# Kernel optimization log

Hardware: AMD Instinct MI355X
Metric: run time of the kernel (lower is better)

The kernel has to match this reference:

```python
import jax, jax.numpy as jnp
import numpy as np

WINDOW_SIZE = 11
SIGMA = 1.5
CHANNEL = 3
L = 2.0
C1 = (0.01 * L) ** 2
C2 = (0.03 * L) ** 2
WEIGHTS = jnp.asarray([0.0448, 0.2856, 0.3001, 0.2363, 0.1333], dtype=jnp.float32)


def _create_window(window_size=WINDOW_SIZE, channel=CHANNEL):
    x = jnp.arange(window_size, dtype=jnp.float32)
    g = jnp.exp(-((x - window_size // 2) ** 2) / (2.0 * SIGMA ** 2))
    g = g / g.sum()
    w2d = jnp.outer(g, g)  # (ws, ws)
    # depthwise kernel, OIHW with I=1, O=channel
    return jnp.broadcast_to(w2d[None, None], (channel, 1, window_size, window_size))


def _depthwise_conv(x, w):
    # x: (B,C,H,W), w: (C,1,kh,kw), groups=C, VALID padding
    return jax.lax.conv_general_dilated(
        x, w, window_strides=(1, 1), padding='VALID',
        feature_group_count=x.shape[1],
        dimension_numbers=('NCHW', 'OIHW', 'NCHW'))


def _ssim_level(img1, img2, window):
    mu1 = _depthwise_conv(img1, window)
    mu2 = _depthwise_conv(img2, window)
    mu1_sq = mu1 * mu1
    mu2_sq = mu2 * mu2
    mu1_mu2 = mu1 * mu2
    sigma1_sq = _depthwise_conv(img1 * img1, window) - mu1_sq
    sigma2_sq = _depthwise_conv(img2 * img2, window) - mu2_sq
    sigma12 = _depthwise_conv(img1 * img2, window) - mu1_mu2
    v1 = 2.0 * sigma12 + C2
    v2 = sigma1_sq + sigma2_sq + C2
    cs = jnp.mean(v1 / v2)
    ssim_map = (2.0 * mu1_mu2 + C1) * v1 / ((mu1_sq + mu2_sq + C1) * v2)
    return jnp.mean(ssim_map), cs


def _avg_pool2(x):
    b, c, h, w = x.shape
    return x.reshape(b, c, h // 2, 2, w // 2, 2).mean(axis=(3, 5))


def _msssim(img1, img2):
    window = _create_window()
    mssim, mcs = [], []
    for _ in range(WEIGHTS.shape[0]):
        sim, cs = _ssim_level(img1, img2, window)
        mssim.append(sim)
        mcs.append(cs)
        img1 = _avg_pool2(img1)
        img2 = _avg_pool2(img2)
    mssim = jnp.stack(mssim)
    mcs = jnp.stack(mcs)
    # normalize=True
    mssim = (mssim + 1.0) / 2.0
    mcs = (mcs + 1.0) / 2.0
    pow1 = mcs ** WEIGHTS
    pow2 = mssim ** WEIGHTS
    # faithful to source: prod over broadcast of pow1[:-1] * pow2[-1]
    return jnp.prod(pow1[:-1] * pow2[-1])


def setup_inputs() -> dict:
    key = jax.random.key(0)
    k1, k2 = jax.random.split(key)
    shape = (16, 3, 512, 512)
    output = jax.random.uniform(k1, shape, dtype=jnp.float32)
    gt = jax.random.uniform(k2, shape, dtype=jnp.float32)
    return {"output": output, "gt": gt}


def reference(output, gt):
    return 1.0 - _msssim(output, gt)
```

## Files before the change

### kernel.cpp

```cpp
#include <hip/hip_runtime.h>
#include <math.h>

typedef float vf2 __attribute__((ext_vector_type(2)));

__device__ __forceinline__ vf2 pk_fma(vf2 a, vf2 b, vf2 c) {
    vf2 d;
    asm("v_pk_fma_f32 %0, %1, %2, %3" : "=v"(d) : "v"(a), "v"(b), "v"(c));
    return d;
}
__device__ __forceinline__ vf2 pk_mul(vf2 a, vf2 b) {
    vf2 d;
    asm("v_pk_mul_f32 %0, %1, %2" : "=v"(d) : "v"(a), "v"(b));
    return d;
}
__device__ __forceinline__ vf2 pk_fma_blo(vf2 w, vf2 b, vf2 c) {
    vf2 d;
    asm("v_pk_fma_f32 %0, %1, %2, %3 op_sel_hi:[0,1,1]"
        : "=v"(d) : "v"(w), "v"(b), "v"(c));
    return d;
}
__device__ __forceinline__ vf2 pk_fma_bhi(vf2 w, vf2 b, vf2 c) {
    vf2 d;
    asm("v_pk_fma_f32 %0, %1, %2, %3 op_sel:[1,0,0] op_sel_hi:[1,1,1]"
        : "=v"(d) : "v"(w), "v"(b), "v"(c));
    return d;
}

#define L0_H 512
#define L0_HOUT 502
#define L0_SEG 64
#define L0_NCHUNK 7
#define ROWW 536
#define NQ 134
#define L0_BUF (11 * ROWW)

#define TILE 32
#define IN_DIM 42
#define SCP 21
#define HALO 10
#define LV_STAGE (IN_DIM * SCP * 4)
#define SH 340
#define HB LV_STAGE
#define MEGA_WORDS (HB + 16 * SH)

__global__ __launch_bounds__(256)
void msssim_cascade(const float* __restrict__ img1, const float* __restrict__ img2,
                    float* __restrict__ Y1, float* __restrict__ Y2,
                    float* __restrict__ Z1, float* __restrict__ Z2,
                    float* __restrict__ W1, float* __restrict__ W2)
{
    __shared__ float xs[16 * 256 * 2];
    __shared__ float ysh[8 * 128 * 2];
    __shared__ float zsh[4 * 64 * 2];
    const int tid = threadIdx.x;
    const int reg = blockIdx.x & 15, plane = blockIdx.x >> 4;
    const long long obase = (long long)plane * 262144;

    for (int i = tid; i < 16 * 256; i += 256) {
        const int r = i >> 8, c = i & 255;
        const long long o = obase + (long long)(2 * (16 * reg + r)) * 512 + 2 * c;
        const float2 a0 = *(const float2*)&img1[o];
        const float2 a1 = *(const float2*)&img1[o + 512];
        const float2 b0 = *(const float2*)&img2[o];
        const float2 b1 = *(const float2*)&img2[o + 512];
        xs[2 * i]     = 0.25f * ((a0.x + b0.x) + (a0.y + b0.y) + (a1.x + b1.x) + (a1.y + b1.y));
        xs[2 * i + 1] = 0.25f * ((a0.x - b0.x) + (a0.y - b0.y) + (a1.x - b1.x) + (a1.y - b1.y));
    }
    __syncthreads();
    for (int i = tid; i < 8 * 128; i += 256) {
        const int r = i >> 7, c = i & 127;
        const int i00 = ((2 * r) * 256 + 2 * c) * 2;
        const float yP = 0.25f * (xs[i00] + xs[i00 + 2] + xs[i00 + 512] + xs[i00 + 514]);
        const float yQ = 0.25f * (xs[i00 + 1] + xs[i00 + 3] + xs[i00 + 513] + xs[i00 + 515]);
        ysh[2 * i] = yP; ysh[2 * i + 1] = yQ;
        const long long yo = (long long)plane * 16384 + (long long)(8 * reg + r) * 128 + c;
        Y1[yo] = yP; Y2[yo] = yQ;
    }
    __syncthreads();
    for (int i = tid; i < 4 * 64; i += 256) {
        const int r = i >> 6, c = i & 63;
        const int i00 = ((2 * r) * 128 + 2 * c) * 2;
        const float zP = 0.25f * (ysh[i00] + ysh[i00 + 2] + ysh[i00 + 256] + ysh[i00 + 258]);
        const float zQ = 0.25f * (ysh[i00 + 1] + ysh[i00 + 3] + ysh[i00 + 257] + ysh[i00 + 259]);
        zsh[2 * i] = zP; zsh[2 * i + 1] = zQ;
        const long long zo = (long long)plane * 4096 + (long long)(4 * reg + r) * 64 + c;
        Z1[zo] = zP; Z2[zo] = zQ;
    }
    __syncthreads();
    for (int i = tid; i < 2 * 32; i += 256) {
        const int r = i >> 5, c = i & 31;
        const int i00 = ((2 * r) * 64 + 2 * c) * 2;
        const long long wo = (long long)plane * 1024 + (long long)(2 * reg + r) * 32 + c;
        W1[wo] = 0.25f * (zsh[i00] + zsh[i00 + 2] + zsh[i00 + 128] + zsh[i00 + 130]);
        W2[wo] = 0.25f * (zsh[i00 + 1] + zsh[i00 + 3] + zsh[i00 + 129] + zsh[i00 + 131]);
    }
}

__global__ __launch_bounds__(256)
void msssim_mega(const float* __restrict__ img1, const float* __restrict__ img2,
                 const float* __restrict__ Y1, const float* __restrict__ Y2,
                 const float* __restrict__ Z1, const float* __restrict__ Z2,
                 const float* __restrict__ W1, const float* __restrict__ W2,
                 double* __restrict__ sums)
{
    __shared__ __align__(16) float smem[MEGA_WORDS];
    __shared__ float wred[4][2];

    const float gs[11] = {0.00102838f, 0.00759875f, 0.03600077f, 0.10936070f,
                          0.21300554f, 0.26601173f, 0.21300554f, 0.10936070f,
                          0.03600077f, 0.00759875f, 0.00102838f};
    const int tid = threadIdx.x;
    const int bid = blockIdx.x;
    const float C1 = 4.0e-4f, C2 = 3.6e-3f;
    float ssim_acc = 0.f, cs_acc = 0.f;
    int level;

    if (bid < 768) {
        level = 0;
        const int c0 = (bid & 1) * 256;
        const int oy0 = ((bid >> 1) & 7) * L0_SEG;
        const long long plane = (long long)(bid >> 4) * 262144;
        const bool colok = (c0 + tid) < L0_HOUT;

        const int par = tid & 1;
        vf2 wp[6];
        #pragma unroll
        for (int jq = 0; jq < 6; ++jq) {
            const int i0 = 2 * jq, i1 = 2 * jq + 1;
            const float we0 = (i0 < 11) ? gs[i0] : 0.f;
            const float wo0 = (i0 >= 1) ? gs[i0 - 1] : 0.f;
            const float we1 = (i1 < 11) ? gs[i1] : 0.f;
            const float wo1 = (i1 >= 1) ? gs[i1 - 1] : 0.f;
            wp[jq].x = par ? wo0 : we0;
            wp[jq].y = par ? wo1 : we1;
        }
        vf2 wgv[6];
        #pragma unroll
        for (int k = 0; k < 6; ++k) { wgv[k].x = gs[k]; wgv[k].y = gs[k]; }

        int rowS[6], colS[6], ldsoff[6], rHS[6];
        #pragma unroll
        for (int t = 0; t < 6; ++t) {
            const int s = tid + 256 * t;
            if (s < 11 * NQ) {
                const int r = s / NQ, q = s - NQ * r;
                rowS[t] = r; colS[t] = c0 + 2 * q;
                ldsoff[t] = r * ROWW + q * 4; rHS[t] = r * L0_H;
            } else { rowS[t] = -1; colS[t] = 0; ldsoff[t] = 0; rHS[t] = 0; }
        }

        float4 pf[6];
        auto prefetch = [&](int ybase) {
            const int yH = ybase * L0_H;
            #pragma unroll
            for (int t = 0; t < 6; ++t) {
                float2 a = make_float2(0.f, 0.f), b = make_float2(0.f, 0.f);
                if (rowS[t] >= 0) {
                    const int y = ybase + rowS[t];
                    if (y < L0_H && colS[t] < L0_H) {
                        const long long idx = plane + yH + rHS[t] + colS[t];
                        a = *(const float2*)(img1 + idx);
                        b = *(const float2*)(img2 + idx);
                    }
                }
                pf[t] = make_float4(a.x + b.x, a.x - b.x, a.y + b.y, a.y - b.y);
            }
        };
        auto stage_write = [&]() {
            #pragma unroll
            for (int t = 0; t < 6; ++t)
                if (rowS[t] >= 0) *(float4*)&smem[ldsoff[t]] = pf[t];
        };

        prefetch(oy0);
        stage_write();
        __syncthreads();

        vf2 pd_pq[11], pd_sq[11];
        #pragma unroll
        for (int s = 0; s < 11; ++s) { pd_pq[s] = (vf2){0.f, 0.f}; pd_sq[s] = (vf2){0.f, 0.f}; }

        const int qb4 = (tid >> 1) * 4;

        for (int c = 0; c < L0_NCHUNK; ++c) {
            const bool more = (c + 1 < L0_NCHUNK);
            if (more) prefetch(oy0 + 11 * (c + 1));

            #pragma unroll
            for (int j = 0; j < 11; ++j) {
                pd_pq[j] = (vf2){0.f, 0.f};
                pd_sq[j] = (vf2){0.f, 0.f};

                float4 q[6];
                const int rw = j * ROWW + qb4;
                #pragma unroll
                for (int u = 0; u < 6; ++u) q[u] = *(const float4*)&smem[rw + 4 * u];

                vf2 hpq = {0.f, 0.f}, hsq = {0.f, 0.f};
                #pragma unroll
                for (int u = 0; u < 6; ++u) {
                    const vf2 elo = {q[u].x, q[u].y};
                    const vf2 ehi = {q[u].z, q[u].w};
                    const vf2 slo = pk_mul(elo, elo);
                    const vf2 shi = pk_mul(ehi, ehi);
                    hpq = pk_fma_blo(wp[u], elo, hpq);
                    hpq = pk_fma_bhi(wp[u], ehi, hpq);
                    hsq = pk_fma_blo(wp[u], slo, hsq);
                    hsq = pk_fma_bhi(wp[u], shi, hsq);
                }
                #pragma unroll
                for (int k = 0; k < 11; ++k) {
                    const int s = (j - k + 11) % 11;
                    const int m = (k <= 5) ? k : 10 - k;
                    pd_pq[s] = pk_fma(wgv[m], hpq, pd_pq[s]);
                    pd_sq[s] = pk_fma(wgv[m], hsq, pd_sq[s]);
                }
                const int yrel = 11 * c + j;
                if (yrel >= 10) {
                    const int s = (j + 1) % 11;
                    const int orow = yrel - 10;
                    if (orow < L0_SEG && (oy0 + orow) < L0_HOUT && colok) {
                        const vf2 musq = pk_mul(pd_pq[s], pd_pq[s]);
                        const float sP = pd_sq[s].x - musq.x;
                        const float sQ = pd_sq[s].y - musq.y;
                        const float v1 = 0.5f * (sP - sQ) + C2;
                        const float v2 = 0.5f * (sP + sQ) + C2;
                        const float num1 = 0.5f * (musq.x - musq.y) + C1;
                        const float den1 = 0.5f * (musq.x + musq.y) + C1;
                        cs_acc += v1 * __builtin_amdgcn_rcpf(v2);
                        ssim_acc += num1 * v1 * __builtin_amdgcn_rcpf(den1 * v2);
                    }
                }
            }

            __syncthreads();
            if (more) stage_write();
            __syncthreads();
        }
    } else {
        const int id = bid - 768;
        const float *src1 = nullptr, *src2 = nullptr;
        int H, strip, seg, plane, tps;
        if (id < 768) {
            level = 1; H = 256; tps = 4;
            plane = id >> 4; const int t = id & 15; strip = t & 7; seg = t >> 3;
        } else if (id < 1536) {
            level = 2; H = 128; tps = 1; src1 = Y1; src2 = Y2;
            const int r = id - 768; plane = r >> 4; const int t = r & 15; strip = t & 3; seg = t >> 2;
        } else if (id < 1728) {
            level = 3; H = 64; tps = 1; src1 = Z1; src2 = Z2;
            const int r = id - 1536; plane = r >> 2; const int t = r & 3; strip = t & 1; seg = t >> 1;
        } else {
            level = 4; H = 32; tps = 1; src1 = W1; src2 = W2;
            plane = id - 1728; strip = 0; seg = 0;
        }

        vf2 wg[11];
        #pragma unroll
        for (int k = 0; k < 11; ++k) { wg[k].x = gs[k]; wg[k].y = gs[k]; }

        const int Hout = H - HALO;
        const int ntiles = (Hout + TILE - 1) / TILE;
        const int tstart = seg * tps;
        const int tend = min(ntiles, tstart + tps);
        const int ox0 = strip * TILE;
        const long long base = (long long)plane * H * H;
        const long long obase = (long long)plane * 262144;

        int rHS[4], rS[4], xS[4];
        #pragma unroll
        for (int t4 = 0; t4 < 4; ++t4) {
            const int s = tid + 256 * t4;
            if (s < IN_DIM * SCP) {
                const int r = s / SCP, cp = s - r * SCP;
                rS[t4] = r; rHS[t4] = r * H; xS[t4] = ox0 + 2 * cp;
            } else { rS[t4] = -1; rHS[t4] = 0; xS[t4] = 0; }
        }

        auto load_slot = [&](int t4, int ybase) -> float4 {
            if (rS[t4] < 0) return make_float4(0.f, 0.f, 0.f, 0.f);
            const int y = ybase + rS[t4], x = xS[t4];
            if (y >= H || x >= H) return make_float4(0.f, 0.f, 0.f, 0.f);
            if (level == 1) {
                const long long o = obase + (long long)(2 * y) * 512 + 2 * x;
                const float4 A0 = *(const float4*)(img1 + o);
                const float4 A1 = *(const float4*)(img1 + o + 512);
                const float4 B0 = *(const float4*)(img2 + o);
                const float4 B1 = *(const float4*)(img2 + o + 512);
                const float P0 = 0.25f * ((A0.x + B0.x) + (A0.y + B0.y) + (A1.x + B1.x) + (A1.y + B1.y));
                const float Q0 = 0.25f * ((A0.x - B0.x) + (A0.y - B0.y) + (A1.x - B1.x) + (A1.y - B1.y));
                const float P1 = 0.25f * ((A0.z + B0.z) + (A0.w + B0.w) + (A1.z + B1.z) + (A1.w + B1.w));
                const float Q1 = 0.25f * ((A0.z - B0.z) + (A0.w - B0.w) + (A1.z - B1.z) + (A1.w - B1.w));
                return make_float4(P0, Q0, P1, Q1);
            }
            const long long idx = base + (long long)ybase * H + rHS[t4] + x;
            const float2 a = *(const float2*)(src1 + idx);
            const float2 b = *(const float2*)(src2 + idx);
            return make_float4(a.x, b.x, a.y, b.y);
        };

        float4 pref[4];
        {
            #pragma unroll
            for (int t4 = 0; t4 < 4; ++t4) pref[t4] = load_slot(t4, tstart * TILE);
            #pragma unroll
            for (int t4 = 0; t4 < 4; ++t4)
                if (rS[t4] >= 0) *(float4*)&smem[(tid + 256 * t4) * 4] = pref[t4];
        }
        __syncthreads();

        for (int tt = tstart; tt < tend; ++tt) {
            const int ty0 = tt * TILE;
            const bool more = (tt + 1 < tend);

            if (more) {
                #pragma unroll
                for (int t4 = 0; t4 < 4; ++t4) pref[t4] = load_slot(t4, ty0 + TILE);
            }

            float4 hA[3], hBv[3];
            #pragma unroll
            for (int t = 0; t < 3; ++t) {
                const int p = tid + 256 * t;
                if (p < IN_DIM * 16) {
                    const int r = p >> 4, m = p & 15;
                    vf2 Apq = {0.f, 0.f}, Asq = {0.f, 0.f};
                    vf2 Bpq = {0.f, 0.f}, Bsq = {0.f, 0.f};
                    #pragma unroll
                    for (int jj = 0; jj < 6; ++jj) {
                        const float4 v = *(const float4*)&smem[(r * SCP + m + jj) * 4];
                        const vf2 lo = {v.x, v.y};
                        const vf2 hi = {v.z, v.w};
                        const vf2 losq = pk_mul(lo, lo);
                        const vf2 hisq = pk_mul(hi, hi);
                        Apq = pk_fma(wg[2 * jj], lo, Apq);
                        Asq = pk_fma(wg[2 * jj], losq, Asq);
                        if (jj >= 1) {
                            Bpq = pk_fma(wg[2 * jj - 1], lo, Bpq);
                            Bsq = pk_fma(wg[2 * jj - 1], losq, Bsq);
                        }
                        if (jj <= 4) {
                            Apq = pk_fma(wg[2 * jj + 1], hi, Apq);
                            Asq = pk_fma(wg[2 * jj + 1], hisq, Asq);
                        }
                        Bpq = pk_fma(wg[2 * jj], hi, Bpq);
                        Bsq = pk_fma(wg[2 * jj], hisq, Bsq);
                    }
                    hA[t]  = make_float4(Apq.x, Apq.y, Asq.x, Asq.y);
                    hBv[t] = make_float4(Bpq.x, Bpq.y, Bsq.x, Bsq.y);
                }
            }
            __syncthreads();

            #pragma unroll
            for (int t = 0; t < 3; ++t) {
                const int p = tid + 256 * t;
                if (p < IN_DIM * 16) {
                    const int r = p >> 4, m = p & 15;
                    const int hb = HB + m * SH + r * 8;
                    *(float4*)&smem[hb]     = hA[t];
                    *(float4*)&smem[hb + 4] = hBv[t];
                }
            }
            if (more) {
                #pragma unroll
                for (int t4 = 0; t4 < 4; ++t4)
                    if (rS[t4] >= 0) *(float4*)&smem[(tid + 256 * t4) * 4] = pref[t4];
            }
            __syncthreads();

            const int tx = tid & 31, rg = tid >> 5;
            const int r0 = rg * 4;
            const int m = tx >> 1, par = tx & 1;
            const int hb = HB + m * SH + par * 4;

            vf2 accPQ[4], accSQ[4];
            #pragma unroll
            for (int o = 0; o < 4; ++o) {
                accPQ[o] = (vf2){0.f, 0.f};
                accSQ[o] = (vf2){0.f, 0.f};
            }
            #pragma unroll
            for (int i = 0; i < 14; ++i) {
                const float4 h4 = *(const float4*)&smem[hb + (r0 + i) * 8];
                const vf2 ppq = {h4.x, h4.y};
                const vf2 psq = {h4.z, h4.w};
                #pragma unroll
                for (int o = 0; o < 4; ++o) {
                    const int k = i - o;
                    if (k >= 0 && k <= 10) {
                        accPQ[o] = pk_fma(wg[k], ppq, accPQ[o]);
                        accSQ[o] = pk_fma(wg[k], psq, accSQ[o]);
                    }
                }
            }

            const int ox = ox0 + tx;
            #pragma unroll
            for (int o = 0; o < 4; ++o) {
                const int oy = ty0 + r0 + o;
                if (oy < Hout && ox < Hout) {
                    const vf2 musq = pk_mul(accPQ[o], accPQ[o]);
                    const float sP = accSQ[o].x - musq.x;
                    const float sQ = accSQ[o].y - musq.y;
                    const float v1 = 0.5f * (sP - sQ) + C2;
                    const float v2 = 0.5f * (sP + sQ) + C2;
                    const float num1 = 0.5f * (musq.x - musq.y) + C1;
                    const float den1 = 0.5f * (musq.x + musq.y) + C1;
                    cs_acc += v1 * __builtin_amdgcn_rcpf(v2);
                    ssim_acc += num1 * v1 * __builtin_amdgcn_rcpf(den1 * v2);
                }
            }
        }
    }

    #pragma unroll
    for (int off = 32; off > 0; off >>= 1) {
        ssim_acc += __shfl_down(ssim_acc, off);
        cs_acc   += __shfl_down(cs_acc, off);
    }
    const int wave = tid >> 6;
    if ((tid & 63) == 0) { wred[wave][0] = ssim_acc; wred[wave][1] = cs_acc; }
    __syncthreads();
    if (tid == 0) {
        const float s = wred[0][0] + wred[1][0] + wred[2][0] + wred[3][0];
        const float c = wred[0][1] + wred[1][1] + wred[2][1] + wred[3][1];
        atomicAdd(&sums[level],     (double)s);
        atomicAdd(&sums[5 + level], (double)c);
    }
}

__global__ void msssim_final_kernel(const double* __restrict__ sums,
                                    float* __restrict__ out)
{
    if (threadIdx.x == 0 && blockIdx.x == 0) {
        const double W[5] = {0.0448, 0.2856, 0.3001, 0.2363, 0.1333};
        const int Houts[5] = {502, 246, 118, 54, 22};
        double mssim[5], mcs[5];
        for (int l = 0; l < 5; ++l) {
            const double cnt = 48.0 * (double)Houts[l] * (double)Houts[l];
            mssim[l] = (sums[l]     / cnt + 1.0) * 0.5;
            mcs[l]   = (sums[5 + l] / cnt + 1.0) * 0.5;
        }
        const double p2 = pow(mssim[4], W[4]);
        double prod = 1.0;
        for (int l = 0; l < 4; ++l) prod *= pow(mcs[l], W[l]) * p2;
        out[0] = (float)(1.0 - prod);
    }
}

extern "C" void kernel_launch(void* const* d_in, const int* in_sizes, int n_in,
                              void* d_out, int out_size, void* d_ws, size_t ws_size,
                              hipStream_t stream)
{
    const float* img1 = (const float*)d_in[0];
    const float* img2 = (const float*)d_in[1];
    float* out = (float*)d_out;
    (void)in_sizes; (void)n_in; (void)out_size; (void)ws_size;

    char* ws = (char*)d_ws;
    double* sums = (double*)ws;
    float* Y1 = (float*)(ws + 256);
    float* Y2 = Y1 + 786432;
    float* Z1 = Y2 + 786432;
    float* Z2 = Z1 + 196608;
    float* W1 = Z2 + 196608;
    float* W2 = W1 + 49152;

    hipMemsetAsync(sums, 0, 10 * sizeof(double), stream);

    hipLaunchKernelGGL(msssim_cascade, dim3(768), dim3(256), 0, stream,
                       img1, img2, Y1, Y2, Z1, Z2, W1, W2);

    hipLaunchKernelGGL(msssim_mega, dim3(2544), dim3(256), 0, stream,
                       img1, img2, Y1, Y2, Z1, Z2, W1, W2, sums);

    hipLaunchKernelGGL(msssim_final_kernel, dim3(1), dim3(64), 0, stream, sums, out);
}
```

Baseline: 129.8 us.

## Materialize level-1 pooled images and process level 1 with streaming row kernel

The cascade kernel now also writes the level-1 pooled P/Q planes (X1/X2) to workspace. The mega kernel's level-1 work then leaves the 32x32 tiled path, which re-pooled from the full-resolution images, and runs through the streaming row-chunk path used for level 0, parameterized by H, Hout and source. This removes redundant full-resolution reads and tile halo overhead for level 1 and cuts the grid size. The cost is an extra ~25MB of global writes and reads for X1/X2, and the prefetch double-buffering in the tiled path is dropped.

```diff
diff --git a/kernel.cpp b/kernel.cpp
--- a/kernel.cpp
+++ b/kernel.cpp
@@ -26,13 +26,11 @@
     return d;
 }
 
-#define L0_H 512
-#define L0_HOUT 502
 #define L0_SEG 64
-#define L0_NCHUNK 7
+#define NCHUNK 7
 #define ROWW 536
 #define NQ 134
-#define L0_BUF (11 * ROWW)
+#define STREAM_BUF (11 * ROWW)
 
 #define TILE 32
 #define IN_DIM 42
@@ -45,6 +43,7 @@
 
 __global__ __launch_bounds__(256)
 void msssim_cascade(const float* __restrict__ img1, const float* __restrict__ img2,
+                    float* __restrict__ X1, float* __restrict__ X2,
                     float* __restrict__ Y1, float* __restrict__ Y2,
                     float* __restrict__ Z1, float* __restrict__ Z2,
                     float* __restrict__ W1, float* __restrict__ W2)
@@ -63,8 +62,11 @@
         const float2 a1 = *(const float2*)&img1[o + 512];
         const float2 b0 = *(const float2*)&img2[o];
         const float2 b1 = *(const float2*)&img2[o + 512];
-        xs[2 * i]     = 0.25f * ((a0.x + b0.x) + (a0.y + b0.y) + (a1.x + b1.x) + (a1.y + b1.y));
-        xs[2 * i + 1] = 0.25f * ((a0.x - b0.x) + (a0.y - b0.y) + (a1.x - b1.x) + (a1.y - b1.y));
+        const float P = 0.25f * ((a0.x + b0.x) + (a0.y + b0.y) + (a1.x + b1.x) + (a1.y + b1.y));
+        const float Q = 0.25f * ((a0.x - b0.x) + (a0.y - b0.y) + (a1.x - b1.x) + (a1.y - b1.y));
+        xs[2 * i] = P; xs[2 * i + 1] = Q;
+        const long long xo = (long long)plane * 65536 + (long long)(16 * reg + r) * 256 + c;
+        X1[xo] = P; X2[xo] = Q;
     }
     __syncthreads();
     for (int i = tid; i < 8 * 128; i += 256) {
@@ -98,6 +100,7 @@
 
 __global__ __launch_bounds__(256)
 void msssim_mega(const float* __restrict__ img1, const float* __restrict__ img2,
+                 const float* __restrict__ X1, const float* __restrict__ X2,
                  const float* __restrict__ Y1, const float* __restrict__ Y2,
                  const float* __restrict__ Z1, const float* __restrict__ Z2,
                  const float* __restrict__ W1, const float* __restrict__ W2,
@@ -115,12 +118,26 @@
     float ssim_acc = 0.f, cs_acc = 0.f;
     int level;
 
-    if (bid < 768) {
-        level = 0;
-        const int c0 = (bid & 1) * 256;
-        const int oy0 = ((bid >> 1) & 7) * L0_SEG;
-        const long long plane = (long long)(bid >> 4) * 262144;
-        const bool colok = (c0 + tid) < L0_HOUT;
+    if (bid < 960) {
+        const float *s1, *s2;
+        int H, Hout, c0, oy0;
+        long long plane;
+        bool pq;
+        if (bid < 768) {
+            level = 0; H = 512; Hout = 502; pq = false;
+            s1 = img1; s2 = img2;
+            c0 = (bid & 1) * 256;
+            oy0 = ((bid >> 1) & 7) * L0_SEG;
+            plane = (long long)(bid >> 4) * 262144;
+        } else {
+            const int id = bid - 768;
+            level = 1; H = 256; Hout = 246; pq = true;
+            s1 = X1; s2 = X2;
+            c0 = 0;
+            oy0 = (id & 3) * L0_SEG;
+            plane = (long long)(id >> 2) * 65536;
+        }
+        const bool colok = (c0 + tid) < Hout;
 
         const int par = tid & 1;
         vf2 wp[6];
@@ -145,25 +162,26 @@
             if (s < 11 * NQ) {
                 const int r = s / NQ, q = s - NQ * r;
                 rowS[t] = r; colS[t] = c0 + 2 * q;
-                ldsoff[t] = r * ROWW + q * 4; rHS[t] = r * L0_H;
+                ldsoff[t] = r * ROWW + q * 4; rHS[t] = r * H;
             } else { rowS[t] = -1; colS[t] = 0; ldsoff[t] = 0; rHS[t] = 0; }
         }
 
         float4 pf[6];
         auto prefetch = [&](int ybase) {
-            const int yH = ybase * L0_H;
+            const long long yH = plane + (long long)ybase * H;
             #pragma unroll
             for (int t = 0; t < 6; ++t) {
                 float2 a = make_float2(0.f, 0.f), b = make_float2(0.f, 0.f);
                 if (rowS[t] >= 0) {
                     const int y = ybase + rowS[t];
-                    if (y < L0_H && colS[t] < L0_H) {
-                        const long long idx = plane + yH + rHS[t] + colS[t];
-                        a = *(const float2*)(img1 + idx);
-                        b = *(const float2*)(img2 + idx);
+                    if (y < H && colS[t] < H) {
+                        const long long idx = yH + rHS[t] + colS[t];
+                        a = *(const float2*)(s1 + idx);
+                        b = *(const float2*)(s2 + idx);
                     }
                 }
-                pf[t] = make_float4(a.x + b.x, a.x - b.x, a.y + b.y, a.y - b.y);
+                pf[t] = pq ? make_float4(a.x, b.x, a.y, b.y)
+                           : make_float4(a.x + b.x, a.x - b.x, a.y + b.y, a.y - b.y);
             }
         };
         auto stage_write = [&]() {
@@ -182,8 +200,8 @@
 
         const int qb4 = (tid >> 1) * 4;
 
-        for (int c = 0; c < L0_NCHUNK; ++c) {
-            const bool more = (c + 1 < L0_NCHUNK);
+        for (int c = 0; c < NCHUNK; ++c) {
+            const bool more = (c + 1 < NCHUNK);
             if (more) prefetch(oy0 + 11 * (c + 1));
 
             #pragma unroll
@@ -219,7 +237,7 @@
                 if (yrel >= 10) {
                     const int s = (j + 1) % 11;
                     const int orow = yrel - 10;
-                    if (orow < L0_SEG && (oy0 + orow) < L0_HOUT && colok) {
+                    if (orow < L0_SEG && (oy0 + orow) < Hout && colok) {
                         const vf2 musq = pk_mul(pd_pq[s], pd_pq[s]);
                         const float sP = pd_sq[s].x - musq.x;
                         const float sQ = pd_sq[s].y - musq.y;
@@ -238,21 +256,18 @@
             __syncthreads();
         }
     } else {
-        const int id = bid - 768;
-        const float *src1 = nullptr, *src2 = nullptr;
-        int H, strip, seg, plane, tps;
+        const int id = bid - 960;
+        const float *src1, *src2;
+        int H, strip, seg, plane;
         if (id < 768) {
-            level = 1; H = 256; tps = 4;
-            plane = id >> 4; const int t = id & 15; strip = t & 7; seg = t >> 3;
-        } else if (id < 1536) {
-            level = 2; H = 128; tps = 1; src1 = Y1; src2 = Y2;
-            const int r = id - 768; plane = r >> 4; const int t = r & 15; strip = t & 3; seg = t >> 2;
-        } else if (id < 1728) {
-            level = 3; H = 64; tps = 1; src1 = Z1; src2 = Z2;
-            const int r = id - 1536; plane = r >> 2; const int t = r & 3; strip = t & 1; seg = t >> 1;
+            level = 2; H = 128; src1 = Y1; src2 = Y2;
+            plane = id >> 4; const int t = id & 15; strip = t & 3; seg = t >> 2;
+        } else if (id < 960) {
+            level = 3; H = 64; src1 = Z1; src2 = Z2;
+            const int r = id - 768; plane = r >> 2; const int t = r & 3; strip = t & 1; seg = t >> 1;
         } else {
-            level = 4; H = 32; tps = 1; src1 = W1; src2 = W2;
-            plane = id - 1728; strip = 0; seg = 0;
+            level = 4; H = 32; src1 = W1; src2 = W2;
+            plane = id - 960; strip = 0; seg = 0;
         }
 
         vf2 wg[11];
@@ -261,11 +276,10 @@
 
         const int Hout = H - HALO;
         const int ntiles = (Hout + TILE - 1) / TILE;
-        const int tstart = seg * tps;
-        const int tend = min(ntiles, tstart + tps);
+        const int tstart = seg;
+        const int tend = min(ntiles, tstart + 1);
         const int ox0 = strip * TILE;
         const long long base = (long long)plane * H * H;
-        const long long obase = (long long)plane * 262144;
 
         int rHS[4], rS[4], xS[4];
         #pragma unroll
@@ -281,18 +295,6 @@
             if (rS[t4] < 0) return make_float4(0.f, 0.f, 0.f, 0.f);
             const int y = ybase + rS[t4], x = xS[t4];
             if (y >= H || x >= H) return make_float4(0.f, 0.f, 0.f, 0.f);
-            if (level == 1) {
-                const long long o = obase + (long long)(2 * y) * 512 + 2 * x;
-                const float4 A0 = *(const float4*)(img1 + o);
-                const float4 A1 = *(const float4*)(img1 + o + 512);
-                const float4 B0 = *(const float4*)(img2 + o);
-                const float4 B1 = *(const float4*)(img2 + o + 512);
-                const float P0 = 0.25f * ((A0.x + B0.x) + (A0.y + B0.y) + (A1.x + B1.x) + (A1.y + B1.y));
-                const float Q0 = 0.25f * ((A0.x - B0.x) + (A0.y - B0.y) + (A1.x - B1.x) + (A1.y - B1.y));
-                const float P1 = 0.25f * ((A0.z + B0.z) + (A0.w + B0.w) + (A1.z + B1.z) + (A1.w + B1.w));
-                const float Q1 = 0.25f * ((A0.z - B0.z) + (A0.w - B0.w) + (A1.z - B1.z) + (A1.w - B1.w));
-                return make_float4(P0, Q0, P1, Q1);
-            }
             const long long idx = base + (long long)ybase * H + rHS[t4] + x;
             const float2 a = *(const float2*)(src1 + idx);
             const float2 b = *(const float2*)(src2 + idx);
@@ -311,12 +313,6 @@
 
         for (int tt = tstart; tt < tend; ++tt) {
             const int ty0 = tt * TILE;
-            const bool more = (tt + 1 < tend);
-
-            if (more) {
-                #pragma unroll
-                for (int t4 = 0; t4 < 4; ++t4) pref[t4] = load_slot(t4, ty0 + TILE);
-            }
 
             float4 hA[3], hBv[3];
             #pragma unroll
@@ -362,11 +358,6 @@
                     *(float4*)&smem[hb + 4] = hBv[t];
                 }
             }
-            if (more) {
-                #pragma unroll
-                for (int t4 = 0; t4 < 4; ++t4)
-                    if (rS[t4] >= 0) *(float4*)&smem[(tid + 256 * t4) * 4] = pref[t4];
-            }
             __syncthreads();
 
             const int tx = tid & 31, rg = tid >> 5;
@@ -460,7 +451,9 @@
 
     char* ws = (char*)d_ws;
     double* sums = (double*)ws;
-    float* Y1 = (float*)(ws + 256);
+    float* X1 = (float*)(ws + 256);
+    float* X2 = X1 + 3145728;
+    float* Y1 = X2 + 3145728;
     float* Y2 = Y1 + 786432;
     float* Z1 = Y2 + 786432;
     float* Z2 = Z1 + 196608;
@@ -470,10 +463,10 @@
     hipMemsetAsync(sums, 0, 10 * sizeof(double), stream);
 
     hipLaunchKernelGGL(msssim_cascade, dim3(768), dim3(256), 0, stream,
-                       img1, img2, Y1, Y2, Z1, Z2, W1, W2);
-
-    hipLaunchKernelGGL(msssim_mega, dim3(2544), dim3(256), 0, stream,
-                       img1, img2, Y1, Y2, Z1, Z2, W1, W2, sums);
+                       img1, img2, X1, X2, Y1, Y2, Z1, Z2, W1, W2);
+
+    hipLaunchKernelGGL(msssim_mega, dim3(1968), dim3(256), 0, stream,
+                       img1, img2, X1, X2, Y1, Y2, Z1, Z2, W1, W2, sums);
 
     hipLaunchKernelGGL(msssim_final_kernel, dim3(1), dim3(64), 0, stream, sums, out);
 }
```

Result: slower. 133.8 us (+3.1%).
